# Optimization experiments

Measured on AMD Instinct MI355X. Metric: run time of the kernel, lower is better.

Reference implementation:

```python
import jax, jax.numpy as jnp
import numpy as np

B, T, H, W, D = 32, 16, 32, 32, 64
N = T * H * W            # num_tokens = 16384
NUM_ELEMENTS = N * D     # world.num_elements
ALPHA = 1.0
EPS = 1e-6


def setup_inputs() -> dict:
    key = jax.random.key(0)
    k1, k2, k3, k4, k5, k6 = jax.random.split(key, 6)
    # uniforms feeding the gumbel noise
    u_g = jax.random.uniform(k1, (B, N), minval=EPS, maxval=1.0 - EPS, dtype=jnp.float32)
    # dirichlet marginal log-probs per axis (matches torch._sample_dirichlet().log())
    logp_t = jnp.log(jax.random.dirichlet(k2, jnp.full((T,), ALPHA), (B,)).astype(jnp.float32))
    logp_h = jnp.log(jax.random.dirichlet(k3, jnp.full((H,), ALPHA), (B,)).astype(jnp.float32))
    logp_w = jnp.log(jax.random.dirichlet(k4, jnp.full((W,), ALPHA), (B,)).astype(jnp.float32))
    # single uniform for the stratified masking rates
    u_k = jax.random.uniform(k5, (1,), dtype=jnp.float32)
    # per-element CRPS score (stand-in for loss_fn(tokens, ensemble), which is external)
    score = jax.random.uniform(k6, (B, N, D), dtype=jnp.float32)
    return {"u_g": u_g, "logp_t": logp_t, "logp_h": logp_h,
            "logp_w": logp_w, "u_k": u_k, "score": score}


def reference(u_g, logp_t, logp_h, logp_w, u_k, score):
    # get_visible_ws: gumbel noise + sum of dirichlet marginals broadcast over (t h w)
    gumbel = -jnp.log(-jnp.log(u_g))                                   # [B, N]
    marg = (logp_t[:, :, None, None]
            + logp_h[:, None, :, None]
            + logp_w[:, None, None, :]).reshape(B, N)                  # [B, N]
    ws = gumbel + marg

    # get_visible_ks: stratified rates -> k per row, clamped to [1, N-1]
    strat = jnp.linspace(0.0, 1.0, B, dtype=ws.dtype)
    rates = (u_k[0] + strat) % 1.0
    ks = jnp.clip((N * rates).astype(jnp.int32), 1, N - 1)             # [B]

    # binary_topk: rank of each token in descending order; visible = rank < k
    order = jnp.argsort(-ws, axis=-1)        # descending argsort        [B, N]
    ranks = jnp.argsort(order, axis=-1)      # inverse permutation       [B, N]
    visible = ranks < ks[:, None]            # bool                      [B, N]

    # masked, rate-corrected loss (land_sea_mask is None branch)
    mask = jnp.broadcast_to(~visible[:, :, None], score.shape).astype(score.dtype)  # [B, N, D]
    rate_correction = jnp.sum(mask, axis=(1, 2), keepdims=True) / NUM_ELEMENTS      # [B, 1, 1]
    loss = jnp.mean(score * mask / rate_correction)
    return loss, visible
```

## Files before the change

### kernel.cpp

```cpp
#include <hip/hip_runtime.h>
#include <hip/hip_bf16.h>

#define B_   32
#define T_   16
#define H_   32
#define W_   32
#define D_   64
#define N_   16384
#define BLK  256
#define BLK_S 1024
#define KPT_S 16
#define LOSS_BLOCKS 2048
#define LOSS_ITERS  16
#define CAP 2048

__global__ __launch_bounds__(BLK_S, 1) void select_kernel(
    const float* __restrict__ u_g,
    const float* __restrict__ logp_t,
    const float* __restrict__ logp_h,
    const float* __restrict__ logp_w,
    const float* __restrict__ u_k,
    float* __restrict__ vis_out,
    double* __restrict__ invrc)
{
    const int b    = blockIdx.x;
    const int tid  = threadIdx.x;
    const int lane = tid & 63;
    const int wv   = tid >> 6;

    __shared__ float s_lt[T_], s_lh[H_], s_lw[W_];
    __shared__ unsigned s_hist[2048];
    __shared__ unsigned s_wsum[16];
    __shared__ int s_bucket, s_above, s_cnt;
    __shared__ unsigned s_thr;
    __shared__ int s_cgt, s_ceq;
    __shared__ unsigned long long s_list[CAP];

    if (tid < T_) s_lt[tid] = logp_t[b*T_ + tid];
    if (tid < H_) s_lh[tid] = logp_h[b*H_ + tid];
    if (tid < W_) s_lw[tid] = logp_w[b*W_ + tid];
    s_hist[tid]        = 0u;
    s_hist[tid + 1024] = 0u;
    if (tid == 0) s_cnt = 0;
    __syncthreads();

    unsigned keys[KPT_S];
#pragma unroll
    for (int i = 0; i < KPT_S; ++i) {
        int   n = i*BLK_S + tid;
        float u = u_g[b*N_ + n];
        float g = -logf(-logf(u));
        int t = n >> 10;
        int h = (n >> 5) & 31;
        int w = n & 31;
        float wsv = g + ((s_lt[t] + s_lh[h]) + s_lw[w]);
        unsigned bits = __float_as_uint(wsv);
        keys[i] = (bits & 0x80000000u) ? ~bits : (bits | 0x80000000u);
        atomicAdd(&s_hist[keys[i] >> 21], 1u);
    }
    __syncthreads();

    float u0    = u_k[0];
    float strat = (b == B_-1) ? 1.0f : (float)((double)b * (1.0/31.0));
    float rate  = fmodf(u0 + strat, 1.0f);
    int   k     = (int)(16384.0f * rate);
    k = k < 1 ? 1 : (k > N_-1 ? N_-1 : k);

    {
        const unsigned h0 = s_hist[2*tid];
        const unsigned h1 = s_hist[2*tid + 1];
        const unsigned p  = h0 + h1;
        unsigned x = p;
#pragma unroll
        for (int off = 1; off < 64; off <<= 1) {
            unsigned y = __shfl_down(x, off);
            if (lane + off < 64) x += y;
        }
        if (lane == 0) s_wsum[wv] = x;
        __syncthreads();
        unsigned wsuf = 0;
#pragma unroll
        for (int w2 = 0; w2 < 16; ++w2) wsuf += (w2 > wv) ? s_wsum[w2] : 0u;
        const unsigned sufExcl = (x - p) + wsuf;
        const unsigned ku = (unsigned)k;
        const unsigned a1 = sufExcl;
        const unsigned a0 = sufExcl + h1;
        if (a1 < ku && ku <= a1 + h1) { s_bucket = 2*tid + 1; s_above = (int)a1; }
        if (a0 < ku && ku <= a0 + h0) { s_bucket = 2*tid;     s_above = (int)a0; }
        __syncthreads();
    }

    const int bucket = s_bucket;
    const int above  = s_above;
    const int need   = k - above;

    s_hist[tid]        = 0u;
    s_hist[tid + 1024] = 0u;
    __syncthreads();
#pragma unroll
    for (int i = 0; i < KPT_S; ++i) {
        if ((int)(keys[i] >> 21) == bucket)
            atomicAdd(&s_hist[(keys[i] >> 10) & 0x7FFu], 1u);
    }
    __syncthreads();

    {
        const unsigned h0 = s_hist[2*tid];
        const unsigned h1 = s_hist[2*tid + 1];
        const unsigned p  = h0 + h1;
        unsigned x = p;
#pragma unroll
        for (int off = 1; off < 64; off <<= 1) {
            unsigned y = __shfl_down(x, off);
            if (lane + off < 64) x += y;
        }
        if (lane == 0) s_wsum[wv] = x;
        __syncthreads();
        unsigned wsuf = 0;
#pragma unroll
        for (int w2 = 0; w2 < 16; ++w2) wsuf += (w2 > wv) ? s_wsum[w2] : 0u;
        const unsigned sufExcl = (x - p) + wsuf;
        const unsigned ku = (unsigned)need;
        const unsigned a1 = sufExcl;
        const unsigned a0 = sufExcl + h1;
        if (a1 < ku && ku <= a1 + h1) { s_bucket = 2*tid + 1; s_above = (int)a1; }
        if (a0 < ku && ku <= a0 + h0) { s_bucket = 2*tid;     s_above = (int)a0; }
        __syncthreads();
    }

    const int bucket2 = s_bucket;
    const int above2  = s_above;
    const int need2   = need - above2;
    const unsigned pfx22 = ((unsigned)bucket << 11) | (unsigned)bucket2;

#pragma unroll
    for (int i = 0; i < KPT_S; ++i) {
        if ((keys[i] >> 10) == pfx22) {
            int slot = atomicAdd(&s_cnt, 1);
            if (slot < CAP)
                s_list[slot] = ((unsigned long long)keys[i] << 32)
                             | (unsigned)(i*BLK_S + tid);
        }
    }
    __syncthreads();

    const int M = s_cnt < CAP ? s_cnt : CAP;
    for (int i = tid; i < M; i += BLK_S) {
        const unsigned ki = (unsigned)(s_list[i] >> 32);
        int gt = 0, eq = 0;
        for (int j = 0; j < M; ++j) {
            const unsigned kj = (unsigned)(s_list[j] >> 32);
            gt += (kj > ki) ? 1 : 0;
            eq += (kj == ki) ? 1 : 0;
        }
        if (gt < need2 && need2 <= gt + eq) {
            s_thr = ki;
            s_cgt = above + above2 + gt;
            s_ceq = eq;
        }
    }
    __syncthreads();

    const unsigned thr = s_thr;
    const int count_gt = s_cgt;
    const int count_eq = s_ceq;
    const int need_eq  = k - count_gt;
    const bool rare    = (count_eq != need_eq);

#pragma unroll
    for (int i = 0; i < KPT_S; ++i) {
        int n = i*BLK_S + tid;
        float v;
        if (keys[i] > thr) {
            v = 1.0f;
        } else if (keys[i] == thr) {
            if (!rare || count_eq > CAP) {
                v = 1.0f;
            } else {
                int rk = 0;
                for (int j = 0; j < M; ++j) {
                    unsigned long long e = s_list[j];
                    rk += ((unsigned)(e >> 32) == thr &&
                           (int)(e & 0xFFFFFFFFull) < n) ? 1 : 0;
                }
                v = (rk < need_eq) ? 1.0f : 0.0f;
            }
        } else {
            v = 0.0f;
        }
        vis_out[b*N_ + n] = v;
    }

    if (tid == 0) {
        float rc = (float)(N_ - k) / (float)N_;
        invrc[b] = 1.0 / (double)rc;
    }
}

__global__ __launch_bounds__(BLK, 1) void loss_kernel(
    const float*  __restrict__ score,
    const float*  __restrict__ vis,
    const double* __restrict__ invrc,
    double*       __restrict__ partial)
{
    const int tid = threadIdx.x;
    __shared__ double s_w[B_];
    if (tid < B_) s_w[tid] = invrc[tid];
    __syncthreads();

    const int gtid = blockIdx.x * BLK + tid;
    const int NT   = LOSS_BLOCKS * BLK;
    const float4* s4 = (const float4*)score;

    float vm[LOSS_ITERS];
#pragma unroll
    for (int i = 0; i < LOSS_ITERS; ++i)
        vm[i] = vis[(gtid + i * NT) >> 4];

    double a = 0.0;
#pragma unroll
    for (int i = 0; i < LOSS_ITERS; ++i) {
        int f = gtid + i * NT;
        if (vm[i] == 0.0f) {
            float4 x = s4[f];
            float  s = (x.x + x.y) + (x.z + x.w);
            a += (double)s * s_w[f >> 18];
        }
    }

    for (int off = 32; off > 0; off >>= 1) a += __shfl_down(a, off);
    __shared__ double s_a[4];
    if ((tid & 63) == 0) s_a[tid >> 6] = a;
    __syncthreads();
    if (tid == 0) partial[blockIdx.x] = s_a[0] + s_a[1] + s_a[2] + s_a[3];
}

__global__ __launch_bounds__(BLK, 1) void finalize_kernel(
    const double* __restrict__ partial,
    float* __restrict__ out)
{
    const int tid = threadIdx.x;
    double t = 0.0;
    for (int i = tid; i < LOSS_BLOCKS; i += BLK) t += partial[i];
    for (int off = 32; off > 0; off >>= 1) t += __shfl_down(t, off);
    __shared__ double s_a[4];
    if ((tid & 63) == 0) s_a[tid >> 6] = t;
    __syncthreads();
    if (tid == 0)
        out[0] = (float)((s_a[0] + s_a[1] + s_a[2] + s_a[3]) / 33554432.0);
}

extern "C" void kernel_launch(void* const* d_in, const int* in_sizes, int n_in,
                              void* d_out, int out_size, void* d_ws, size_t ws_size,
                              hipStream_t stream) {
    const float* u_g    = (const float*)d_in[0];
    const float* logp_t = (const float*)d_in[1];
    const float* logp_h = (const float*)d_in[2];
    const float* logp_w = (const float*)d_in[3];
    const float* u_k    = (const float*)d_in[4];
    const float* score  = (const float*)d_in[5];

    float*  out     = (float*)d_out;
    double* wsd     = (double*)d_ws;
    double* invrc   = wsd;
    double* partial = wsd + B_;

    select_kernel<<<B_, BLK_S, 0, stream>>>(u_g, logp_t, logp_h, logp_w, u_k,
                                            out + 1, invrc);
    loss_kernel<<<LOSS_BLOCKS, BLK, 0, stream>>>(score, out + 1, invrc, partial);
    finalize_kernel<<<1, BLK, 0, stream>>>(partial, out);
}
```

Measured before the change: 35.29 us.

## Split selection into parallel key/histogram pass and fuse finalize into loss kernel

The single 32-block selection kernel is split in two. First a 256-block kernel computes the gumbel keys and per-segment first-level histograms, writing the keys into the output buffer. Then a 32-block kernel merges the histograms and does the refinement and threshold steps. The separate finalize launch is removed: the loss kernel now does a last-block reduction through an atomic counter. The aim is to spread the transcendental key computation across more of the GPU and drop one launch, at the cost of an extra global round trip for the keys and histograms.

```diff
diff --git a/kernel.cpp b/kernel.cpp
--- a/kernel.cpp
+++ b/kernel.cpp
@@ -9,45 +9,42 @@
 #define N_   16384
 #define BLK  256
 #define BLK_S 1024
+#define SEG_  8
+#define KPT_A 2
 #define KPT_S 16
 #define LOSS_BLOCKS 2048
 #define LOSS_ITERS  16
 #define CAP 2048
-
-__global__ __launch_bounds__(BLK_S, 1) void select_kernel(
+#define NBIN 2048
+
+__global__ __launch_bounds__(BLK_S, 1) void select_a_kernel(
     const float* __restrict__ u_g,
     const float* __restrict__ logp_t,
     const float* __restrict__ logp_h,
     const float* __restrict__ logp_w,
-    const float* __restrict__ u_k,
-    float* __restrict__ vis_out,
-    double* __restrict__ invrc)
+    unsigned* __restrict__ keys_out,
+    unsigned* __restrict__ hist_out,
+    int* __restrict__ counter)
 {
-    const int b    = blockIdx.x;
-    const int tid  = threadIdx.x;
-    const int lane = tid & 63;
-    const int wv   = tid >> 6;
+    const int ba  = blockIdx.x;
+    const int b   = ba >> 3;
+    const int sg  = ba & 7;
+    const int tid = threadIdx.x;
 
     __shared__ float s_lt[T_], s_lh[H_], s_lw[W_];
-    __shared__ unsigned s_hist[2048];
-    __shared__ unsigned s_wsum[16];
-    __shared__ int s_bucket, s_above, s_cnt;
-    __shared__ unsigned s_thr;
-    __shared__ int s_cgt, s_ceq;
-    __shared__ unsigned long long s_list[CAP];
-
+    __shared__ unsigned s_hist[NBIN];
+
+    if (ba == 0 && tid == 0) *counter = 0;
     if (tid < T_) s_lt[tid] = logp_t[b*T_ + tid];
     if (tid < H_) s_lh[tid] = logp_h[b*H_ + tid];
     if (tid < W_) s_lw[tid] = logp_w[b*W_ + tid];
     s_hist[tid]        = 0u;
     s_hist[tid + 1024] = 0u;
-    if (tid == 0) s_cnt = 0;
-    __syncthreads();
-
-    unsigned keys[KPT_S];
-#pragma unroll
-    for (int i = 0; i < KPT_S; ++i) {
-        int   n = i*BLK_S + tid;
+    __syncthreads();
+
+#pragma unroll
+    for (int i = 0; i < KPT_A; ++i) {
+        int   n = sg*(N_/SEG_) + i*BLK_S + tid;
         float u = u_g[b*N_ + n];
         float g = -logf(-logf(u));
         int t = n >> 10;
@@ -55,10 +52,52 @@
         int w = n & 31;
         float wsv = g + ((s_lt[t] + s_lh[h]) + s_lw[w]);
         unsigned bits = __float_as_uint(wsv);
-        keys[i] = (bits & 0x80000000u) ? ~bits : (bits | 0x80000000u);
-        atomicAdd(&s_hist[keys[i] >> 21], 1u);
-    }
-    __syncthreads();
+        unsigned key  = (bits & 0x80000000u) ? ~bits : (bits | 0x80000000u);
+        keys_out[b*N_ + n] = key;
+        atomicAdd(&s_hist[key >> 21], 1u);
+    }
+    __syncthreads();
+
+    hist_out[ba*NBIN + tid]        = s_hist[tid];
+    hist_out[ba*NBIN + tid + 1024] = s_hist[tid + 1024];
+}
+
+__global__ __launch_bounds__(BLK_S, 1) void select_b_kernel(
+    unsigned* keybuf,
+    const unsigned* __restrict__ hist_in,
+    const float* __restrict__ u_k,
+    double* __restrict__ invrc)
+{
+    const int b    = blockIdx.x;
+    const int tid  = threadIdx.x;
+    const int lane = tid & 63;
+    const int wv   = tid >> 6;
+
+    __shared__ unsigned s_hist2[NBIN];
+    __shared__ unsigned s_wsum[16];
+    __shared__ int s_bucket, s_above, s_cnt;
+    __shared__ unsigned s_thr;
+    __shared__ int s_cgt, s_ceq;
+    __shared__ unsigned long long s_list[CAP];
+
+    s_hist2[tid]        = 0u;
+    s_hist2[tid + 1024] = 0u;
+    if (tid == 0) s_cnt = 0;
+
+    unsigned h0 = 0, h1 = 0;
+    {
+        const uint2* hb2 = (const uint2*)(hist_in + (size_t)b*SEG_*NBIN);
+#pragma unroll
+        for (int j = 0; j < SEG_; ++j) {
+            uint2 v = hb2[j*(NBIN/2) + tid];
+            h0 += v.x; h1 += v.y;
+        }
+    }
+
+    unsigned keys[KPT_S];
+#pragma unroll
+    for (int i = 0; i < KPT_S; ++i)
+        keys[i] = keybuf[b*N_ + i*BLK_S + tid];
 
     float u0    = u_k[0];
     float strat = (b == B_-1) ? 1.0f : (float)((double)b * (1.0/31.0));
@@ -67,9 +106,7 @@
     k = k < 1 ? 1 : (k > N_-1 ? N_-1 : k);
 
     {
-        const unsigned h0 = s_hist[2*tid];
-        const unsigned h1 = s_hist[2*tid + 1];
-        const unsigned p  = h0 + h1;
+        const unsigned p = h0 + h1;
         unsigned x = p;
 #pragma unroll
         for (int off = 1; off < 64; off <<= 1) {
@@ -94,20 +131,17 @@
     const int above  = s_above;
     const int need   = k - above;
 
-    s_hist[tid]        = 0u;
-    s_hist[tid + 1024] = 0u;
-    __syncthreads();
 #pragma unroll
     for (int i = 0; i < KPT_S; ++i) {
         if ((int)(keys[i] >> 21) == bucket)
-            atomicAdd(&s_hist[(keys[i] >> 10) & 0x7FFu], 1u);
+            atomicAdd(&s_hist2[(keys[i] >> 10) & 0x7FFu], 1u);
     }
     __syncthreads();
 
     {
-        const unsigned h0 = s_hist[2*tid];
-        const unsigned h1 = s_hist[2*tid + 1];
-        const unsigned p  = h0 + h1;
+        const unsigned g0 = s_hist2[2*tid];
+        const unsigned g1 = s_hist2[2*tid + 1];
+        const unsigned p  = g0 + g1;
         unsigned x = p;
 #pragma unroll
         for (int off = 1; off < 64; off <<= 1) {
@@ -122,9 +156,9 @@
         const unsigned sufExcl = (x - p) + wsuf;
         const unsigned ku = (unsigned)need;
         const unsigned a1 = sufExcl;
-        const unsigned a0 = sufExcl + h1;
-        if (a1 < ku && ku <= a1 + h1) { s_bucket = 2*tid + 1; s_above = (int)a1; }
-        if (a0 < ku && ku <= a0 + h0) { s_bucket = 2*tid;     s_above = (int)a0; }
+        const unsigned a0 = sufExcl + g1;
+        if (a1 < ku && ku <= a1 + g1) { s_bucket = 2*tid + 1; s_above = (int)a1; }
+        if (a0 < ku && ku <= a0 + g0) { s_bucket = 2*tid;     s_above = (int)a0; }
         __syncthreads();
     }
 
@@ -188,7 +222,7 @@
         } else {
             v = 0.0f;
         }
-        vis_out[b*N_ + n] = v;
+        keybuf[b*N_ + n] = __float_as_uint(v);
     }
 
     if (tid == 0) {
@@ -201,7 +235,9 @@
     const float*  __restrict__ score,
     const float*  __restrict__ vis,
     const double* __restrict__ invrc,
-    double*       __restrict__ partial)
+    double*       __restrict__ partial,
+    int*          __restrict__ counter,
+    float*        __restrict__ out)
 {
     const int tid = threadIdx.x;
     __shared__ double s_w[B_];
@@ -230,24 +266,26 @@
 
     for (int off = 32; off > 0; off >>= 1) a += __shfl_down(a, off);
     __shared__ double s_a[4];
+    __shared__ int s_last;
     if ((tid & 63) == 0) s_a[tid >> 6] = a;
     __syncthreads();
-    if (tid == 0) partial[blockIdx.x] = s_a[0] + s_a[1] + s_a[2] + s_a[3];
-}
-
-__global__ __launch_bounds__(BLK, 1) void finalize_kernel(
-    const double* __restrict__ partial,
-    float* __restrict__ out)
-{
-    const int tid = threadIdx.x;
-    double t = 0.0;
-    for (int i = tid; i < LOSS_BLOCKS; i += BLK) t += partial[i];
-    for (int off = 32; off > 0; off >>= 1) t += __shfl_down(t, off);
-    __shared__ double s_a[4];
-    if ((tid & 63) == 0) s_a[tid >> 6] = t;
-    __syncthreads();
-    if (tid == 0)
-        out[0] = (float)((s_a[0] + s_a[1] + s_a[2] + s_a[3]) / 33554432.0);
+    if (tid == 0) {
+        partial[blockIdx.x] = s_a[0] + s_a[1] + s_a[2] + s_a[3];
+        __threadfence();
+        int prev = atomicAdd(counter, 1);
+        s_last = (prev == LOSS_BLOCKS - 1) ? 1 : 0;
+    }
+    __syncthreads();
+    if (s_last) {
+        __threadfence();
+        double t = 0.0;
+        for (int i = tid; i < LOSS_BLOCKS; i += BLK) t += partial[i];
+        for (int off = 32; off > 0; off >>= 1) t += __shfl_down(t, off);
+        if ((tid & 63) == 0) s_a[tid >> 6] = t;
+        __syncthreads();
+        if (tid == 0)
+            out[0] = (float)((s_a[0] + s_a[1] + s_a[2] + s_a[3]) / 33554432.0);
+    }
 }
 
 extern "C" void kernel_launch(void* const* d_in, const int* in_sizes, int n_in,
@@ -262,11 +300,15 @@
 
     float*  out     = (float*)d_out;
     double* wsd     = (double*)d_ws;
-    double* invrc   = wsd;
-    double* partial = wsd + B_;
-
-    select_kernel<<<B_, BLK_S, 0, stream>>>(u_g, logp_t, logp_h, logp_w, u_k,
-                                            out + 1, invrc);
-    loss_kernel<<<LOSS_BLOCKS, BLK, 0, stream>>>(score, out + 1, invrc, partial);
-    finalize_kernel<<<1, BLK, 0, stream>>>(partial, out);
+    double*   invrc   = wsd;
+    double*   partial = wsd + B_;
+    int*      counter = (int*)(wsd + B_ + LOSS_BLOCKS);
+    unsigned* histbuf = (unsigned*)(wsd + B_ + LOSS_BLOCKS + 8);
+    unsigned* keybuf  = (unsigned*)(out + 1);
+
+    select_a_kernel<<<B_*SEG_, BLK_S, 0, stream>>>(u_g, logp_t, logp_h, logp_w,
+                                                   keybuf, histbuf, counter);
+    select_b_kernel<<<B_, BLK_S, 0, stream>>>(keybuf, histbuf, u_k, invrc);
+    loss_kernel<<<LOSS_BLOCKS, BLK, 0, stream>>>(score, (const float*)keybuf,
+                                                 invrc, partial, counter, out);
 }
```

Measured after the change: 84.11 us. 138% more time.
